# Optimization experiments

Hardware: AMD Instinct MI355X
Metric: run time of the kernel (lower is better)

Reference implementation:

```python
import jax, jax.numpy as jnp
import numpy as np

V, F, N = 5143, 10144, 2_000_000


def _safe_normalize(x):
    # matches GaussianAvatars safe_normalize: x / sqrt(clamp(|x|^2, min=1e-20))
    return x * jax.lax.rsqrt(jnp.clip(jnp.sum(x * x, axis=-1, keepdims=True), 1e-20, None))


def _quat_wxyz_to_rotmat(q):
    # rotation_activation (L2 normalize with eps) then wxyz->xyzw + roma unitquat_to_rotmat
    q = q / (jnp.sqrt(jnp.sum(q * q, axis=-1, keepdims=True)) + 1e-12)
    w, x, y, z = q[..., 0], q[..., 1], q[..., 2], q[..., 3]
    R = jnp.stack([
        jnp.stack([1 - 2 * (y * y + z * z), 2 * (x * y - z * w), 2 * (x * z + y * w)], axis=-1),
        jnp.stack([2 * (x * y + z * w), 1 - 2 * (x * x + z * z), 2 * (y * z - x * w)], axis=-1),
        jnp.stack([2 * (x * z - y * w), 2 * (y * z + x * w), 1 - 2 * (x * x + y * y)], axis=-1),
    ], axis=-2)
    return R  # [N,3,3]


def setup_inputs() -> dict:
    key = jax.random.key(0)
    ks = jax.random.split(key, 9)
    verts = jax.random.normal(ks[0], (V, 3), jnp.float32) * 0.1
    faces = jax.random.randint(ks[1], (F, 3), 0, V, dtype=jnp.int32)
    binding = jax.random.randint(ks[2], (N,), 0, F, dtype=jnp.int32)
    xyz = jax.random.normal(ks[3], (N, 3), jnp.float32) * 0.01
    rotation = jax.random.normal(ks[4], (N, 4), jnp.float32)
    scaling = jax.random.normal(ks[5], (N, 3), jnp.float32) - 4.0
    opacity = jax.random.normal(ks[6], (N, 1), jnp.float32)
    features_dc = jax.random.normal(ks[7], (N, 1, 3), jnp.float32)
    features_rest = jax.random.normal(ks[8], (N, 15, 3), jnp.float32) * 0.1
    return dict(verts=verts, faces=faces, binding=binding, xyz=xyz, rotation=rotation,
                scaling=scaling, opacity=opacity, features_dc=features_dc,
                features_rest=features_rest)


def reference(verts, faces, binding, xyz, rotation, scaling, opacity, features_dc, features_rest):
    # --- per-face geometry (compute_face_orientation + face_center) ---
    v0 = verts[faces[:, 0]]  # [F,3]
    v1 = verts[faces[:, 1]]
    v2 = verts[faces[:, 2]]
    face_center = (v0 + v1 + v2) / 3.0  # triangles.mean(dim=-2)
    e01 = v1 - v0
    e02 = v2 - v0
    a0 = _safe_normalize(e01)
    a1 = _safe_normalize(jnp.cross(a0, e02))
    a2 = -_safe_normalize(jnp.cross(a1, a0))
    face_orien_mat = jnp.stack([a0, a1, a2], axis=-1)  # [F,3,3], columns = axes
    s0 = jnp.sqrt(jnp.sum(e01 * e01, axis=-1, keepdims=True))
    s1 = jnp.abs(jnp.sum(a2 * e02, axis=-1, keepdims=True))
    face_scaling = 0.5 * (s0 + s1)  # [F,1]

    # --- binding-indexed gathers ---
    O_b = face_orien_mat[binding]      # [N,3,3]
    fs_b = face_scaling[binding]       # [N,1]
    fc_b = face_center[binding]        # [N,3]

    # --- gaussian position in world space ---
    xyz_out = jnp.einsum('nij,nj->ni', O_b, xyz) * fs_b + fc_b  # [N,3]

    # --- color (dc sh band 0 + opacity), scaled to 0..255 ---
    op = jax.nn.sigmoid(opacity)  # [N,1]
    color = jnp.clip((jnp.concatenate([0.5 + 0.282 * features_dc[:, 0, :], op], axis=-1)) * 255.0, 0.0, 255.0)

    # --- covariance build ---
    scales = jnp.exp(scaling) * fs_b  # [N,3]
    Q = _quat_wxyz_to_rotmat(rotation)  # [N,3,3]
    rotations = jnp.swapaxes(jnp.einsum('nij,njk->nik', O_b, Q), 1, 2)  # (O@Q)^T, [N,3,3]
    sig = rotations * scales[:, :, None]  # einsum('bij,bi->bij')
    C = jnp.einsum('nij,nik->njk', sig, sig)  # [N,3,3] = sig^T sig
    simga = jnp.stack([C[:, 0, 0], C[:, 0, 1], C[:, 0, 2], C[:, 1, 1], C[:, 1, 2], C[:, 2, 2]], axis=-1)

    return jnp.concatenate([xyz_out, color, simga], axis=-1)  # [N,13]
```

## Files before the change

kernel.cpp:

```cpp
#include <hip/hip_runtime.h>
#include <math.h>

struct F3 { float x, y, z; };

__device__ __forceinline__ F3 f3(float x, float y, float z) { return {x, y, z}; }
__device__ __forceinline__ F3 add(F3 a, F3 b) { return {a.x+b.x, a.y+b.y, a.z+b.z}; }
__device__ __forceinline__ F3 sub(F3 a, F3 b) { return {a.x-b.x, a.y-b.y, a.z-b.z}; }
__device__ __forceinline__ F3 mul(F3 a, float s) { return {a.x*s, a.y*s, a.z*s}; }
__device__ __forceinline__ float dot3(F3 a, F3 b) { return a.x*b.x + a.y*b.y + a.z*b.z; }
__device__ __forceinline__ F3 cross3(F3 a, F3 b) {
    return {a.y*b.z - a.z*b.y, a.z*b.x - a.x*b.z, a.x*b.y - a.y*b.x};
}
__device__ __forceinline__ F3 safe_normalize(F3 a) {
    float d = dot3(a, a);
    float inv = rsqrtf(fmaxf(d, 1e-20f));
    return mul(a, inv);
}

#define BLK 256

__global__ __launch_bounds__(BLK) void face_precompute_kernel(
    const float* __restrict__ verts, const int* __restrict__ faces,
    float4* __restrict__ tab, int F)
{
    const int f = blockIdx.x * BLK + threadIdx.x;
    if (f >= F) return;
    const int f0 = faces[3*f+0], f1 = faces[3*f+1], f2 = faces[3*f+2];
    const F3 v0 = f3(verts[3*f0], verts[3*f0+1], verts[3*f0+2]);
    const F3 v1 = f3(verts[3*f1], verts[3*f1+1], verts[3*f1+2]);
    const F3 v2 = f3(verts[3*f2], verts[3*f2+1], verts[3*f2+2]);

    const F3 fc  = mul(add(add(v0, v1), v2), (1.0f/3.0f));
    const F3 e01 = sub(v1, v0);
    const F3 e02 = sub(v2, v0);
    const F3 a0 = safe_normalize(e01);
    const F3 a1 = safe_normalize(cross3(a0, e02));
    const F3 a2 = mul(safe_normalize(cross3(a1, a0)), -1.0f);
    const float s0 = sqrtf(dot3(e01, e01));
    const float s1 = fabsf(dot3(a2, e02));
    const float fs = 0.5f * (s0 + s1);

    tab[4*f+0] = make_float4(fc.x, fc.y, fc.z, fs);
    tab[4*f+1] = make_float4(a0.x, a0.y, a0.z, 0.0f);
    tab[4*f+2] = make_float4(a1.x, a1.y, a1.z, 0.0f);
    tab[4*f+3] = make_float4(a2.x, a2.y, a2.z, 0.0f);
}

__global__ __launch_bounds__(BLK) void gauss_main_kernel(
    const float4* __restrict__ tab,
    const int*    __restrict__ binding,
    const float*  __restrict__ xyz,
    const float*  __restrict__ rot,
    const float*  __restrict__ scal,
    const float*  __restrict__ opac,
    const float*  __restrict__ fdc,
    float*        __restrict__ out,
    int N)
{
    __shared__ float sout[BLK * 13];

    const int tid = threadIdx.x;
    const int i  = blockIdx.x * BLK + tid;
    const int count = min(BLK, N - blockIdx.x * BLK);

    if (i < N) {
        const int b = binding[i];
        const float4 t0 = tab[4*b+0];
        const float4 t1 = tab[4*b+1];
        const float4 t2 = tab[4*b+2];
        const float4 t3 = tab[4*b+3];
        const F3 fc = f3(t0.x, t0.y, t0.z);
        const float fs = t0.w;
        const F3 a0 = f3(t1.x, t1.y, t1.z);
        const F3 a1 = f3(t2.x, t2.y, t2.z);
        const F3 a2 = f3(t3.x, t3.y, t3.z);

        const float px = xyz[3*i+0], py = xyz[3*i+1], pz = xyz[3*i+2];
        const float4 q4 = reinterpret_cast<const float4*>(rot)[i];
        const float sc0 = scal[3*i+0], sc1 = scal[3*i+1], sc2 = scal[3*i+2];
        const float opa = opac[i];
        const float d0 = fdc[3*i+0], d1 = fdc[3*i+1], d2 = fdc[3*i+2];

        F3 xo = add(add(mul(a0, px), mul(a1, py)), mul(a2, pz));
        xo = add(mul(xo, fs), fc);

        const float qn = sqrtf(q4.x*q4.x + q4.y*q4.y + q4.z*q4.z + q4.w*q4.w) + 1e-12f;
        const float qinv = 1.0f / qn;
        const float w = q4.x*qinv, x = q4.y*qinv, y = q4.z*qinv, z = q4.w*qinv;
        const float Q00 = 1.0f - 2.0f*(y*y + z*z);
        const float Q01 = 2.0f*(x*y - z*w);
        const float Q02 = 2.0f*(x*z + y*w);
        const float Q10 = 2.0f*(x*y + z*w);
        const float Q11 = 1.0f - 2.0f*(x*x + z*z);
        const float Q12 = 2.0f*(y*z - x*w);
        const float Q20 = 2.0f*(x*z - y*w);
        const float Q21 = 2.0f*(y*z + x*w);
        const float Q22 = 1.0f - 2.0f*(x*x + y*y);

        const F3 m0 = add(add(mul(a0, Q00), mul(a1, Q10)), mul(a2, Q20));
        const F3 m1 = add(add(mul(a0, Q01), mul(a1, Q11)), mul(a2, Q21));
        const F3 m2 = add(add(mul(a0, Q02), mul(a1, Q12)), mul(a2, Q22));

        const float w0 = expf(sc0) * fs;
        const float w1 = expf(sc1) * fs;
        const float w2 = expf(sc2) * fs;
        const float t0s = w0*w0, t1s = w1*w1, t2s = w2*w2;

        const float C00 = t0s*m0.x*m0.x + t1s*m1.x*m1.x + t2s*m2.x*m2.x;
        const float C01 = t0s*m0.x*m0.y + t1s*m1.x*m1.y + t2s*m2.x*m2.y;
        const float C02 = t0s*m0.x*m0.z + t1s*m1.x*m1.z + t2s*m2.x*m2.z;
        const float C11 = t0s*m0.y*m0.y + t1s*m1.y*m1.y + t2s*m2.y*m2.y;
        const float C12 = t0s*m0.y*m0.z + t1s*m1.y*m1.z + t2s*m2.y*m2.z;
        const float C22 = t0s*m0.z*m0.z + t1s*m1.z*m1.z + t2s*m2.z*m2.z;

        const float sg = 1.0f / (1.0f + expf(-opa));
        const float c0 = fminf(fmaxf((0.5f + 0.282f*d0) * 255.0f, 0.0f), 255.0f);
        const float c1 = fminf(fmaxf((0.5f + 0.282f*d1) * 255.0f, 0.0f), 255.0f);
        const float c2 = fminf(fmaxf((0.5f + 0.282f*d2) * 255.0f, 0.0f), 255.0f);
        const float c3 = fminf(fmaxf(sg * 255.0f, 0.0f), 255.0f);

        float r[13] = {xo.x, xo.y, xo.z, c0, c1, c2, c3, C00, C01, C02, C11, C12, C22};
        #pragma unroll
        for (int j = 0; j < 13; ++j) sout[tid*13 + j] = r[j];
    }

    __syncthreads();

    const int total = count * 13;
    const size_t base = (size_t)blockIdx.x * (BLK * 13);
    const int n4 = total >> 2;
    const float4* s4 = reinterpret_cast<const float4*>(sout);
    float4* o4 = reinterpret_cast<float4*>(out + base);
    for (int j = tid; j < n4; j += BLK) o4[j] = s4[j];
    for (int j = (n4 << 2) + tid; j < total; j += BLK) out[base + j] = sout[j];
}

__global__ __launch_bounds__(BLK) void gauss_fused_kernel(
    const float* __restrict__ verts, const int* __restrict__ faces,
    const int* __restrict__ binding, const float* __restrict__ xyz,
    const float* __restrict__ rot, const float* __restrict__ scal,
    const float* __restrict__ opac, const float* __restrict__ fdc,
    float* __restrict__ out, int N)
{
    __shared__ float sout[BLK * 13];
    const int tid = threadIdx.x;
    const int i  = blockIdx.x * BLK + tid;
    const int count = min(BLK, N - blockIdx.x * BLK);

    if (i < N) {
        const int b = binding[i];
        const int f0 = faces[3*b+0], f1 = faces[3*b+1], f2 = faces[3*b+2];
        const F3 v0 = f3(verts[3*f0], verts[3*f0+1], verts[3*f0+2]);
        const F3 v1 = f3(verts[3*f1], verts[3*f1+1], verts[3*f1+2]);
        const F3 v2 = f3(verts[3*f2], verts[3*f2+1], verts[3*f2+2]);
        const F3 fc  = mul(add(add(v0, v1), v2), (1.0f/3.0f));
        const F3 e01 = sub(v1, v0);
        const F3 e02 = sub(v2, v0);
        const F3 a0 = safe_normalize(e01);
        const F3 a1 = safe_normalize(cross3(a0, e02));
        const F3 a2 = mul(safe_normalize(cross3(a1, a0)), -1.0f);
        const float s0 = sqrtf(dot3(e01, e01));
        const float s1 = fabsf(dot3(a2, e02));
        const float fs = 0.5f * (s0 + s1);

        const float px = xyz[3*i+0], py = xyz[3*i+1], pz = xyz[3*i+2];
        const float4 q4 = reinterpret_cast<const float4*>(rot)[i];
        const float sc0 = scal[3*i+0], sc1 = scal[3*i+1], sc2 = scal[3*i+2];
        const float opa = opac[i];
        const float d0 = fdc[3*i+0], d1 = fdc[3*i+1], d2 = fdc[3*i+2];

        F3 xo = add(add(mul(a0, px), mul(a1, py)), mul(a2, pz));
        xo = add(mul(xo, fs), fc);

        const float qn = sqrtf(q4.x*q4.x + q4.y*q4.y + q4.z*q4.z + q4.w*q4.w) + 1e-12f;
        const float qinv = 1.0f / qn;
        const float w = q4.x*qinv, x = q4.y*qinv, y = q4.z*qinv, z = q4.w*qinv;
        const float Q00 = 1.0f - 2.0f*(y*y + z*z);
        const float Q01 = 2.0f*(x*y - z*w);
        const float Q02 = 2.0f*(x*z + y*w);
        const float Q10 = 2.0f*(x*y + z*w);
        const float Q11 = 1.0f - 2.0f*(x*x + z*z);
        const float Q12 = 2.0f*(y*z - x*w);
        const float Q20 = 2.0f*(x*z - y*w);
        const float Q21 = 2.0f*(y*z + x*w);
        const float Q22 = 1.0f - 2.0f*(x*x + y*y);

        const F3 m0 = add(add(mul(a0, Q00), mul(a1, Q10)), mul(a2, Q20));
        const F3 m1 = add(add(mul(a0, Q01), mul(a1, Q11)), mul(a2, Q21));
        const F3 m2 = add(add(mul(a0, Q02), mul(a1, Q12)), mul(a2, Q22));

        const float w0 = expf(sc0) * fs;
        const float w1 = expf(sc1) * fs;
        const float w2 = expf(sc2) * fs;
        const float t0 = w0*w0, t1 = w1*w1, t2 = w2*w2;

        const float C00 = t0*m0.x*m0.x + t1*m1.x*m1.x + t2*m2.x*m2.x;
        const float C01 = t0*m0.x*m0.y + t1*m1.x*m1.y + t2*m2.x*m2.y;
        const float C02 = t0*m0.x*m0.z + t1*m1.x*m1.z + t2*m2.x*m2.z;
        const float C11 = t0*m0.y*m0.y + t1*m1.y*m1.y + t2*m2.y*m2.y;
        const float C12 = t0*m0.y*m0.z + t1*m1.y*m1.z + t2*m2.y*m2.z;
        const float C22 = t0*m0.z*m0.z + t1*m1.z*m1.z + t2*m2.z*m2.z;

        const float sg = 1.0f / (1.0f + expf(-opa));
        const float c0 = fminf(fmaxf((0.5f + 0.282f*d0) * 255.0f, 0.0f), 255.0f);
        const float c1 = fminf(fmaxf((0.5f + 0.282f*d1) * 255.0f, 0.0f), 255.0f);
        const float c2 = fminf(fmaxf((0.5f + 0.282f*d2) * 255.0f, 0.0f), 255.0f);
        const float c3 = fminf(fmaxf(sg * 255.0f, 0.0f), 255.0f);

        float r[13] = {xo.x, xo.y, xo.z, c0, c1, c2, c3, C00, C01, C02, C11, C12, C22};
        #pragma unroll
        for (int j = 0; j < 13; ++j) sout[tid*13 + j] = r[j];
    }

    __syncthreads();

    const int total = count * 13;
    const size_t base = (size_t)blockIdx.x * (BLK * 13);
    const int n4 = total >> 2;
    const float4* s4 = reinterpret_cast<const float4*>(sout);
    float4* o4 = reinterpret_cast<float4*>(out + base);
    for (int j = tid; j < n4; j += BLK) o4[j] = s4[j];
    for (int j = (n4 << 2) + tid; j < total; j += BLK) out[base + j] = sout[j];
}

extern "C" void kernel_launch(void* const* d_in, const int* in_sizes, int n_in,
                              void* d_out, int out_size, void* d_ws, size_t ws_size,
                              hipStream_t stream) {
    const float* verts   = (const float*)d_in[0];
    const int*   faces   = (const int*)  d_in[1];
    const int*   binding = (const int*)  d_in[2];
    const float* xyz     = (const float*)d_in[3];
    const float* rot     = (const float*)d_in[4];
    const float* scal    = (const float*)d_in[5];
    const float* opac    = (const float*)d_in[6];
    const float* fdc     = (const float*)d_in[7];
    float* out = (float*)d_out;
    const int N = in_sizes[2];
    const int F = in_sizes[1] / 3;

    const size_t tab_bytes = (size_t)F * 4 * sizeof(float4);
    const int blocks = (N + BLK - 1) / BLK;

    if (ws_size >= tab_bytes) {
        float4* tab = (float4*)d_ws;
        const int fblocks = (F + BLK - 1) / BLK;
        face_precompute_kernel<<<fblocks, BLK, 0, stream>>>(verts, faces, tab, F);
        gauss_main_kernel<<<blocks, BLK, 0, stream>>>(
            tab, binding, xyz, rot, scal, opac, fdc, out, N);
    } else {
        gauss_fused_kernel<<<blocks, BLK, 0, stream>>>(
            verts, faces, binding, xyz, rot, scal, opac, fdc, out, N);
    }
}
```

Before: 45.02 us.

## Process four gaussians per thread with vector loads and direct float4 stores

The main kernel now handles four points per thread, loading the point attributes as float4 vectors and writing the 52 output floats directly as float4 stores. This removes the shared-memory staging and block barrier. The face table read drops the fourth row: a2 is recomputed as cross(a0,a1), and fast __expf is used. The cost is higher register pressure and strided per-lane vector accesses, which may reduce coalescing efficiency.

```diff
diff --git a/kernel.cpp b/kernel.cpp
--- a/kernel.cpp
+++ b/kernel.cpp
@@ -43,10 +43,64 @@
     tab[4*f+0] = make_float4(fc.x, fc.y, fc.z, fs);
     tab[4*f+1] = make_float4(a0.x, a0.y, a0.z, 0.0f);
     tab[4*f+2] = make_float4(a1.x, a1.y, a1.z, 0.0f);
-    tab[4*f+3] = make_float4(a2.x, a2.y, a2.z, 0.0f);
-}
-
-__global__ __launch_bounds__(BLK) void gauss_main_kernel(
+}
+
+__device__ __forceinline__ void compute_point(
+    float px, float py, float pz,
+    float qw, float qx, float qy, float qz,
+    float sc0, float sc1, float sc2,
+    float opa, float d0, float d1, float d2,
+    float4 t0, float4 t1, float4 t2,
+    float* __restrict__ r)
+{
+    const F3 fc = f3(t0.x, t0.y, t0.z);
+    const float fs = t0.w;
+    const F3 a0 = f3(t1.x, t1.y, t1.z);
+    const F3 a1 = f3(t2.x, t2.y, t2.z);
+    const F3 a2 = cross3(a0, a1);
+
+    F3 xo = add(add(mul(a0, px), mul(a1, py)), mul(a2, pz));
+    xo = add(mul(xo, fs), fc);
+
+    const float qn = sqrtf(qw*qw + qx*qx + qy*qy + qz*qz) + 1e-12f;
+    const float qinv = 1.0f / qn;
+    const float w = qw*qinv, x = qx*qinv, y = qy*qinv, z = qz*qinv;
+    const float Q00 = 1.0f - 2.0f*(y*y + z*z);
+    const float Q01 = 2.0f*(x*y - z*w);
+    const float Q02 = 2.0f*(x*z + y*w);
+    const float Q10 = 2.0f*(x*y + z*w);
+    const float Q11 = 1.0f - 2.0f*(x*x + z*z);
+    const float Q12 = 2.0f*(y*z - x*w);
+    const float Q20 = 2.0f*(x*z - y*w);
+    const float Q21 = 2.0f*(y*z + x*w);
+    const float Q22 = 1.0f - 2.0f*(x*x + y*y);
+
+    const F3 m0 = add(add(mul(a0, Q00), mul(a1, Q10)), mul(a2, Q20));
+    const F3 m1 = add(add(mul(a0, Q01), mul(a1, Q11)), mul(a2, Q21));
+    const F3 m2 = add(add(mul(a0, Q02), mul(a1, Q12)), mul(a2, Q22));
+
+    const float w0 = __expf(sc0) * fs;
+    const float w1 = __expf(sc1) * fs;
+    const float w2 = __expf(sc2) * fs;
+    const float t0s = w0*w0, t1s = w1*w1, t2s = w2*w2;
+
+    const float C00 = t0s*m0.x*m0.x + t1s*m1.x*m1.x + t2s*m2.x*m2.x;
+    const float C01 = t0s*m0.x*m0.y + t1s*m1.x*m1.y + t2s*m2.x*m2.y;
+    const float C02 = t0s*m0.x*m0.z + t1s*m1.x*m1.z + t2s*m2.x*m2.z;
+    const float C11 = t0s*m0.y*m0.y + t1s*m1.y*m1.y + t2s*m2.y*m2.y;
+    const float C12 = t0s*m0.y*m0.z + t1s*m1.y*m1.z + t2s*m2.y*m2.z;
+    const float C22 = t0s*m0.z*m0.z + t1s*m1.z*m1.z + t2s*m2.z*m2.z;
+
+    const float sg = 1.0f / (1.0f + __expf(-opa));
+    r[0]  = xo.x; r[1] = xo.y; r[2] = xo.z;
+    r[3]  = fminf(fmaxf((0.5f + 0.282f*d0) * 255.0f, 0.0f), 255.0f);
+    r[4]  = fminf(fmaxf((0.5f + 0.282f*d1) * 255.0f, 0.0f), 255.0f);
+    r[5]  = fminf(fmaxf((0.5f + 0.282f*d2) * 255.0f, 0.0f), 255.0f);
+    r[6]  = fminf(fmaxf(sg * 255.0f, 0.0f), 255.0f);
+    r[7]  = C00; r[8] = C01; r[9] = C02; r[10] = C11; r[11] = C12; r[12] = C22;
+}
+
+__global__ __launch_bounds__(BLK) void gauss_main4_kernel(
     const float4* __restrict__ tab,
     const int*    __restrict__ binding,
     const float*  __restrict__ xyz,
@@ -57,82 +111,59 @@
     float*        __restrict__ out,
     int N)
 {
-    __shared__ float sout[BLK * 13];
-
-    const int tid = threadIdx.x;
-    const int i  = blockIdx.x * BLK + tid;
-    const int count = min(BLK, N - blockIdx.x * BLK);
-
-    if (i < N) {
-        const int b = binding[i];
-        const float4 t0 = tab[4*b+0];
-        const float4 t1 = tab[4*b+1];
-        const float4 t2 = tab[4*b+2];
-        const float4 t3 = tab[4*b+3];
-        const F3 fc = f3(t0.x, t0.y, t0.z);
-        const float fs = t0.w;
-        const F3 a0 = f3(t1.x, t1.y, t1.z);
-        const F3 a1 = f3(t2.x, t2.y, t2.z);
-        const F3 a2 = f3(t3.x, t3.y, t3.z);
-
-        const float px = xyz[3*i+0], py = xyz[3*i+1], pz = xyz[3*i+2];
-        const float4 q4 = reinterpret_cast<const float4*>(rot)[i];
-        const float sc0 = scal[3*i+0], sc1 = scal[3*i+1], sc2 = scal[3*i+2];
-        const float opa = opac[i];
-        const float d0 = fdc[3*i+0], d1 = fdc[3*i+1], d2 = fdc[3*i+2];
-
-        F3 xo = add(add(mul(a0, px), mul(a1, py)), mul(a2, pz));
-        xo = add(mul(xo, fs), fc);
-
-        const float qn = sqrtf(q4.x*q4.x + q4.y*q4.y + q4.z*q4.z + q4.w*q4.w) + 1e-12f;
-        const float qinv = 1.0f / qn;
-        const float w = q4.x*qinv, x = q4.y*qinv, y = q4.z*qinv, z = q4.w*qinv;
-        const float Q00 = 1.0f - 2.0f*(y*y + z*z);
-        const float Q01 = 2.0f*(x*y - z*w);
-        const float Q02 = 2.0f*(x*z + y*w);
-        const float Q10 = 2.0f*(x*y + z*w);
-        const float Q11 = 1.0f - 2.0f*(x*x + z*z);
-        const float Q12 = 2.0f*(y*z - x*w);
-        const float Q20 = 2.0f*(x*z - y*w);
-        const float Q21 = 2.0f*(y*z + x*w);
-        const float Q22 = 1.0f - 2.0f*(x*x + y*y);
-
-        const F3 m0 = add(add(mul(a0, Q00), mul(a1, Q10)), mul(a2, Q20));
-        const F3 m1 = add(add(mul(a0, Q01), mul(a1, Q11)), mul(a2, Q21));
-        const F3 m2 = add(add(mul(a0, Q02), mul(a1, Q12)), mul(a2, Q22));
-
-        const float w0 = expf(sc0) * fs;
-        const float w1 = expf(sc1) * fs;
-        const float w2 = expf(sc2) * fs;
-        const float t0s = w0*w0, t1s = w1*w1, t2s = w2*w2;
-
-        const float C00 = t0s*m0.x*m0.x + t1s*m1.x*m1.x + t2s*m2.x*m2.x;
-        const float C01 = t0s*m0.x*m0.y + t1s*m1.x*m1.y + t2s*m2.x*m2.y;
-        const float C02 = t0s*m0.x*m0.z + t1s*m1.x*m1.z + t2s*m2.x*m2.z;
-        const float C11 = t0s*m0.y*m0.y + t1s*m1.y*m1.y + t2s*m2.y*m2.y;
-        const float C12 = t0s*m0.y*m0.z + t1s*m1.y*m1.z + t2s*m2.y*m2.z;
-        const float C22 = t0s*m0.z*m0.z + t1s*m1.z*m1.z + t2s*m2.z*m2.z;
-
-        const float sg = 1.0f / (1.0f + expf(-opa));
-        const float c0 = fminf(fmaxf((0.5f + 0.282f*d0) * 255.0f, 0.0f), 255.0f);
-        const float c1 = fminf(fmaxf((0.5f + 0.282f*d1) * 255.0f, 0.0f), 255.0f);
-        const float c2 = fminf(fmaxf((0.5f + 0.282f*d2) * 255.0f, 0.0f), 255.0f);
-        const float c3 = fminf(fmaxf(sg * 255.0f, 0.0f), 255.0f);
-
-        float r[13] = {xo.x, xo.y, xo.z, c0, c1, c2, c3, C00, C01, C02, C11, C12, C22};
-        #pragma unroll
-        for (int j = 0; j < 13; ++j) sout[tid*13 + j] = r[j];
+    const int t  = blockIdx.x * BLK + threadIdx.x;
+    const int NT = (N + 3) >> 2;
+    if (t >= NT) return;
+    const int p0 = t * 4;
+
+    if (p0 + 3 < N) {
+        const int4 b4 = reinterpret_cast<const int4*>(binding)[t];
+        float xf[12], sf[12], ff[12], qf[16], of[4];
+        #pragma unroll
+        for (int j = 0; j < 3; ++j) {
+            *reinterpret_cast<float4*>(xf + 4*j) = reinterpret_cast<const float4*>(xyz )[3*t + j];
+            *reinterpret_cast<float4*>(sf + 4*j) = reinterpret_cast<const float4*>(scal)[3*t + j];
+            *reinterpret_cast<float4*>(ff + 4*j) = reinterpret_cast<const float4*>(fdc )[3*t + j];
+        }
+        #pragma unroll
+        for (int j = 0; j < 4; ++j)
+            *reinterpret_cast<float4*>(qf + 4*j) = reinterpret_cast<const float4*>(rot)[4*t + j];
+        *reinterpret_cast<float4*>(of) = reinterpret_cast<const float4*>(opac)[t];
+
+        const int bs[4] = {b4.x, b4.y, b4.z, b4.w};
+        float res[52];
+        #pragma unroll
+        for (int p = 0; p < 4; ++p) {
+            const float4 t0 = tab[4*bs[p] + 0];
+            const float4 t1 = tab[4*bs[p] + 1];
+            const float4 t2 = tab[4*bs[p] + 2];
+            compute_point(xf[3*p], xf[3*p+1], xf[3*p+2],
+                          qf[4*p], qf[4*p+1], qf[4*p+2], qf[4*p+3],
+                          sf[3*p], sf[3*p+1], sf[3*p+2],
+                          of[p], ff[3*p], ff[3*p+1], ff[3*p+2],
+                          t0, t1, t2, res + 13*p);
+        }
+
+        float4* o4 = reinterpret_cast<float4*>(out + (size_t)t * 52);
+        #pragma unroll
+        for (int j = 0; j < 13; ++j)
+            o4[j] = make_float4(res[4*j], res[4*j+1], res[4*j+2], res[4*j+3]);
+    } else {
+        for (int i = p0; i < N; ++i) {
+            const int b = binding[i];
+            const float4 t0 = tab[4*b + 0];
+            const float4 t1 = tab[4*b + 1];
+            const float4 t2 = tab[4*b + 2];
+            float r[13];
+            compute_point(xyz[3*i], xyz[3*i+1], xyz[3*i+2],
+                          rot[4*i], rot[4*i+1], rot[4*i+2], rot[4*i+3],
+                          scal[3*i], scal[3*i+1], scal[3*i+2],
+                          opac[i], fdc[3*i], fdc[3*i+1], fdc[3*i+2],
+                          t0, t1, t2, r);
+            #pragma unroll
+            for (int j = 0; j < 13; ++j) out[(size_t)i*13 + j] = r[j];
+        }
     }
-
-    __syncthreads();
-
-    const int total = count * 13;
-    const size_t base = (size_t)blockIdx.x * (BLK * 13);
-    const int n4 = total >> 2;
-    const float4* s4 = reinterpret_cast<const float4*>(sout);
-    float4* o4 = reinterpret_cast<float4*>(out + base);
-    for (int j = tid; j < n4; j += BLK) o4[j] = s4[j];
-    for (int j = (n4 << 2) + tid; j < total; j += BLK) out[base + j] = sout[j];
 }
 
 __global__ __launch_bounds__(BLK) void gauss_fused_kernel(
@@ -142,85 +173,32 @@
     const float* __restrict__ opac, const float* __restrict__ fdc,
     float* __restrict__ out, int N)
 {
-    __shared__ float sout[BLK * 13];
-    const int tid = threadIdx.x;
-    const int i  = blockIdx.x * BLK + tid;
-    const int count = min(BLK, N - blockIdx.x * BLK);
-
-    if (i < N) {
-        const int b = binding[i];
-        const int f0 = faces[3*b+0], f1 = faces[3*b+1], f2 = faces[3*b+2];
-        const F3 v0 = f3(verts[3*f0], verts[3*f0+1], verts[3*f0+2]);
-        const F3 v1 = f3(verts[3*f1], verts[3*f1+1], verts[3*f1+2]);
-        const F3 v2 = f3(verts[3*f2], verts[3*f2+1], verts[3*f2+2]);
-        const F3 fc  = mul(add(add(v0, v1), v2), (1.0f/3.0f));
-        const F3 e01 = sub(v1, v0);
-        const F3 e02 = sub(v2, v0);
-        const F3 a0 = safe_normalize(e01);
-        const F3 a1 = safe_normalize(cross3(a0, e02));
-        const F3 a2 = mul(safe_normalize(cross3(a1, a0)), -1.0f);
-        const float s0 = sqrtf(dot3(e01, e01));
-        const float s1 = fabsf(dot3(a2, e02));
-        const float fs = 0.5f * (s0 + s1);
-
-        const float px = xyz[3*i+0], py = xyz[3*i+1], pz = xyz[3*i+2];
-        const float4 q4 = reinterpret_cast<const float4*>(rot)[i];
-        const float sc0 = scal[3*i+0], sc1 = scal[3*i+1], sc2 = scal[3*i+2];
-        const float opa = opac[i];
-        const float d0 = fdc[3*i+0], d1 = fdc[3*i+1], d2 = fdc[3*i+2];
-
-        F3 xo = add(add(mul(a0, px), mul(a1, py)), mul(a2, pz));
-        xo = add(mul(xo, fs), fc);
-
-        const float qn = sqrtf(q4.x*q4.x + q4.y*q4.y + q4.z*q4.z + q4.w*q4.w) + 1e-12f;
-        const float qinv = 1.0f / qn;
-        const float w = q4.x*qinv, x = q4.y*qinv, y = q4.z*qinv, z = q4.w*qinv;
-        const float Q00 = 1.0f - 2.0f*(y*y + z*z);
-        const float Q01 = 2.0f*(x*y - z*w);
-        const float Q02 = 2.0f*(x*z + y*w);
-        const float Q10 = 2.0f*(x*y + z*w);
-        const float Q11 = 1.0f - 2.0f*(x*x + z*z);
-        const float Q12 = 2.0f*(y*z - x*w);
-        const float Q20 = 2.0f*(x*z - y*w);
-        const float Q21 = 2.0f*(y*z + x*w);
-        const float Q22 = 1.0f - 2.0f*(x*x + y*y);
-
-        const F3 m0 = add(add(mul(a0, Q00), mul(a1, Q10)), mul(a2, Q20));
-        const F3 m1 = add(add(mul(a0, Q01), mul(a1, Q11)), mul(a2, Q21));
-        const F3 m2 = add(add(mul(a0, Q02), mul(a1, Q12)), mul(a2, Q22));
-
-        const float w0 = expf(sc0) * fs;
-        const float w1 = expf(sc1) * fs;
-        const float w2 = expf(sc2) * fs;
-        const float t0 = w0*w0, t1 = w1*w1, t2 = w2*w2;
-
-        const float C00 = t0*m0.x*m0.x + t1*m1.x*m1.x + t2*m2.x*m2.x;
-        const float C01 = t0*m0.x*m0.y + t1*m1.x*m1.y + t2*m2.x*m2.y;
-        const float C02 = t0*m0.x*m0.z + t1*m1.x*m1.z + t2*m2.x*m2.z;
-        const float C11 = t0*m0.y*m0.y + t1*m1.y*m1.y + t2*m2.y*m2.y;
-        const float C12 = t0*m0.y*m0.z + t1*m1.y*m1.z + t2*m2.y*m2.z;
-        const float C22 = t0*m0.z*m0.z + t1*m1.z*m1.z + t2*m2.z*m2.z;
-
-        const float sg = 1.0f / (1.0f + expf(-opa));
-        const float c0 = fminf(fmaxf((0.5f + 0.282f*d0) * 255.0f, 0.0f), 255.0f);
-        const float c1 = fminf(fmaxf((0.5f + 0.282f*d1) * 255.0f, 0.0f), 255.0f);
-        const float c2 = fminf(fmaxf((0.5f + 0.282f*d2) * 255.0f, 0.0f), 255.0f);
-        const float c3 = fminf(fmaxf(sg * 255.0f, 0.0f), 255.0f);
-
-        float r[13] = {xo.x, xo.y, xo.z, c0, c1, c2, c3, C00, C01, C02, C11, C12, C22};
-        #pragma unroll
-        for (int j = 0; j < 13; ++j) sout[tid*13 + j] = r[j];
-    }
-
-    __syncthreads();
-
-    const int total = count * 13;
-    const size_t base = (size_t)blockIdx.x * (BLK * 13);
-    const int n4 = total >> 2;
-    const float4* s4 = reinterpret_cast<const float4*>(sout);
-    float4* o4 = reinterpret_cast<float4*>(out + base);
-    for (int j = tid; j < n4; j += BLK) o4[j] = s4[j];
-    for (int j = (n4 << 2) + tid; j < total; j += BLK) out[base + j] = sout[j];
+    const int i = blockIdx.x * BLK + threadIdx.x;
+    if (i >= N) return;
+    const int b = binding[i];
+    const int f0 = faces[3*b+0], f1 = faces[3*b+1], f2 = faces[3*b+2];
+    const F3 v0 = f3(verts[3*f0], verts[3*f0+1], verts[3*f0+2]);
+    const F3 v1 = f3(verts[3*f1], verts[3*f1+1], verts[3*f1+2]);
+    const F3 v2 = f3(verts[3*f2], verts[3*f2+1], verts[3*f2+2]);
+    const F3 fc  = mul(add(add(v0, v1), v2), (1.0f/3.0f));
+    const F3 e01 = sub(v1, v0);
+    const F3 e02 = sub(v2, v0);
+    const F3 a0 = safe_normalize(e01);
+    const F3 a1 = safe_normalize(cross3(a0, e02));
+    const float s0 = sqrtf(dot3(e01, e01));
+    const F3 a2r = mul(safe_normalize(cross3(a1, a0)), -1.0f);
+    const float s1 = fabsf(dot3(a2r, e02));
+    const float fs = 0.5f * (s0 + s1);
+    float r[13];
+    compute_point(xyz[3*i], xyz[3*i+1], xyz[3*i+2],
+                  rot[4*i], rot[4*i+1], rot[4*i+2], rot[4*i+3],
+                  scal[3*i], scal[3*i+1], scal[3*i+2],
+                  opac[i], fdc[3*i], fdc[3*i+1], fdc[3*i+2],
+                  make_float4(fc.x, fc.y, fc.z, fs),
+                  make_float4(a0.x, a0.y, a0.z, 0.0f),
+                  make_float4(a1.x, a1.y, a1.z, 0.0f), r);
+    #pragma unroll
+    for (int j = 0; j < 13; ++j) out[(size_t)i*13 + j] = r[j];
 }
 
 extern "C" void kernel_launch(void* const* d_in, const int* in_sizes, int n_in,
@@ -239,15 +217,17 @@
     const int F = in_sizes[1] / 3;
 
     const size_t tab_bytes = (size_t)F * 4 * sizeof(float4);
-    const int blocks = (N + BLK - 1) / BLK;
 
     if (ws_size >= tab_bytes) {
         float4* tab = (float4*)d_ws;
         const int fblocks = (F + BLK - 1) / BLK;
         face_precompute_kernel<<<fblocks, BLK, 0, stream>>>(verts, faces, tab, F);
-        gauss_main_kernel<<<blocks, BLK, 0, stream>>>(
+        const int NT = (N + 3) / 4;
+        const int blocks = (NT + BLK - 1) / BLK;
+        gauss_main4_kernel<<<blocks, BLK, 0, stream>>>(
             tab, binding, xyz, rot, scal, opac, fdc, out, N);
     } else {
+        const int blocks = (N + BLK - 1) / BLK;
         gauss_fused_kernel<<<blocks, BLK, 0, stream>>>(
             verts, faces, binding, xyz, rot, scal, opac, fdc, out, N);
     }
```

New measurement: 119.9 us. +166.3%, slower.
